# Optimization experiments

Measured on AMD Instinct MI355X. Metric: run time of the kernel, lower is better.

## Reference

```python
import jax, jax.numpy as jnp
import numpy as np

TEMPERATURE = 0.1
EPS = 1e-12  # F.normalize eps


def setup_inputs() -> dict:
    key = jax.random.key(0)
    k1, k2 = jax.random.split(key)
    B, D = 4096, 128
    return {
        "x_i": jax.random.normal(k1, (B, D), dtype=jnp.float32),
        "x_j": jax.random.normal(k2, (B, D), dtype=jnp.float32),
    }


def _l2_normalize(x):
    n = jnp.sqrt(jnp.sum(x * x, axis=1, keepdims=True))
    return x / jnp.maximum(n, EPS)


def reference(x_i, x_j):
    B = x_i.shape[0]
    z = jnp.concatenate([_l2_normalize(x_i), _l2_normalize(x_j)], axis=0)  # [2B, D]
    # cosine similarity of unit-norm rows == dot product -> single GEMM
    sim = z @ z.T  # [2B, 2B]
    idx = jnp.arange(B)
    sim_ij = sim[idx, idx + B]   # diag(sim, +B)
    sim_ji = sim[idx + B, idx]   # diag(sim, -B)
    positives = jnp.concatenate([sim_ij, sim_ji], axis=0)  # [2B]
    neg_mask = 1.0 - jnp.eye(2 * B, dtype=sim.dtype)
    denominator = jnp.sum(neg_mask * jnp.exp(sim / TEMPERATURE), axis=1)  # [2B]
    # -log(exp(pos/t) / denom) = -(pos/t - log denom)
    loss_partial = jnp.log(denominator) - positives / TEMPERATURE
    return jnp.sum(loss_partial) / (2 * B)
```

## Files before the change

### kernel.cpp

```cpp
#include <hip/hip_runtime.h>
#include <stdint.h>

#define D_DIM 128
#define NROW 8192
#define L2EPS 1e-12f
#define SCALE_A 14.426950408889634f
#define LN2 0.6931471805599453f
#define NPART 50

typedef __attribute__((ext_vector_type(4))) int   i32x4;
typedef __attribute__((ext_vector_type(8))) int   i32x8;
typedef __attribute__((ext_vector_type(4))) float f32x4;

#define AS1 __attribute__((address_space(1)))
#define AS3 __attribute__((address_space(3)))

static __device__ inline void gload_lds16(const void* g, void* l) {
    __builtin_amdgcn_global_load_lds((const AS1 uint32_t*)g, (AS3 uint32_t*)l, 16, 0, 0);
}

static __device__ inline i32x8 cat8(i32x4 lo, i32x4 hi) {
    i32x8 r;
    r[0] = lo[0]; r[1] = lo[1]; r[2] = lo[2]; r[3] = lo[3];
    r[4] = hi[0]; r[5] = hi[1]; r[6] = hi[2]; r[7] = hi[3];
    return r;
}

__global__ __launch_bounds__(256) void k_normalize(
        const float* __restrict__ xi, const float* __restrict__ xj,
        uint8_t* __restrict__ z8, uint8_t* __restrict__ z8s,
        float* __restrict__ pos_acc, float* __restrict__ logsum,
        unsigned* __restrict__ done_ct) {
    const int wave = threadIdx.x >> 6;
    const int lane = threadIdx.x & 63;
    const int row = blockIdx.x * 4 + wave;
    const float* src = (row < 4096) ? (xi + (size_t)row * D_DIM)
                                    : (xj + (size_t)(row - 4096) * D_DIM);
    float2 v = *(const float2*)(src + lane * 2);
    float ss = v.x * v.x + v.y * v.y;
#pragma unroll
    for (int m = 32; m >= 1; m >>= 1) ss += __shfl_xor(ss, m, 64);
    const float scale = 1.0f / fmaxf(sqrtf(ss), L2EPS);
    const float scale_a = scale * SCALE_A;
    const int pk_b = __builtin_amdgcn_cvt_pk_fp8_f32(v.x * scale,   v.y * scale,   0, false);
    const int pk_a = __builtin_amdgcn_cvt_pk_fp8_f32(v.x * scale_a, v.y * scale_a, 0, false);
    *(ushort*)(z8  + (size_t)row * D_DIM + lane * 2) = (ushort)pk_b;
    *(ushort*)(z8s + (size_t)row * D_DIM + lane * 2) = (ushort)pk_a;

    if (blockIdx.x == 0 && threadIdx.x == 0) {
        pos_acc[0] = 0.0f; logsum[0] = 0.0f; done_ct[0] = 0u;
    }
}

__global__ __launch_bounds__(256) void k_gemm(
        const uint8_t* __restrict__ z8, const uint8_t* __restrict__ z8s,
        float* __restrict__ part, float* __restrict__ pos_acc) {
    __shared__ __align__(16) uint8_t lds[32768];

    const int t = threadIdx.x;
    const int wave = t >> 6, lane = t & 63;
    const int quad = lane >> 4, lc = lane & 15;

    const int mb = blockIdx.x >> 6;
    const int rb = blockIdx.x & 63;
    const int rowbase = rb * 128;
    const bool diag = (mb == 16);
    const int c1 = diag ? rb : (rb + 2 * mb + 1) & 63;
    const int c2 = (rb + 2 * mb + 2) & 63;

    {
        const uint8_t* zb1 = z8 + (size_t)c1 * 128 * D_DIM;
#pragma unroll
        for (int q = 0; q < 4; q++) {
            const int s = q * 256 + t;
            const int r = s >> 3;
            const int g = (s & 7) ^ (r & 7);
            gload_lds16(zb1 + (size_t)r * D_DIM + g * 16, &lds[s * 16]);
        }
        if (!diag) {
            const uint8_t* zb2 = z8 + (size_t)c2 * 128 * D_DIM;
#pragma unroll
            for (int q = 0; q < 4; q++) {
                const int s = q * 256 + t;
                const int r = s >> 3;
                const int g = (s & 7) ^ (r & 7);
                gload_lds16(zb2 + (size_t)r * D_DIM + g * 16, &lds[16384 + s * 16]);
            }
        }
    }

    i32x8 afr[2];
    {
        const uint8_t* pa = z8s + (size_t)(rowbase + wave * 32 + lc) * D_DIM + quad * 32;
#pragma unroll
        for (int i = 0; i < 2; i++) {
            i32x4 lo = *(const i32x4*)(pa + i * 16 * D_DIM);
            i32x4 hi = *(const i32x4*)(pa + i * 16 * D_DIM + 16);
            afr[i] = cat8(lo, hi);
        }
    }

    asm volatile("s_waitcnt vmcnt(0)" ::: "memory");
    __syncthreads();

    float rs[2][4] = {{0.f,0.f,0.f,0.f},{0.f,0.f,0.f,0.f}};
    float cs[16];
#pragma unroll
    for (int j = 0; j < 16; j++) cs[j] = 0.f;
    float posp = 0.f;
    const int rl0 = wave * 32 + quad * 4;

#define MFMA_J(j, A0, A1)                                                     \
    i32x4 blo, bhi; {                                                         \
        const int rowb = ((j) * 16 + lc) * D_DIM;                             \
        blo = *(const i32x4*)&lds[rowb + (((quad * 2)     ^ (lc & 7)) * 16)]; \
        bhi = *(const i32x4*)&lds[rowb + (((quad * 2 + 1) ^ (lc & 7)) * 16)]; \
    }                                                                         \
    const i32x8 bfr = cat8(blo, bhi);                                         \
    f32x4 z4 = {0.f, 0.f, 0.f, 0.f};                                          \
    f32x4 A0 = __builtin_amdgcn_mfma_scale_f32_16x16x128_f8f6f4(              \
                   afr[0], bfr, z4, 0, 0, 0, 127, 0, 127);                    \
    f32x4 A1 = __builtin_amdgcn_mfma_scale_f32_16x16x128_f8f6f4(              \
                   afr[1], bfr, z4, 0, 0, 0, 127, 0, 127);

    if (!diag) {
#pragma unroll
        for (int j = 0; j < 8; j++) {
            MFMA_J(j, a0, a1)
#pragma unroll
            for (int r = 0; r < 4; r++) {
                const float e0 = exp2f(a0[r]);
                const float e1 = exp2f(a1[r]);
                rs[0][r] += e0;
                rs[1][r] += e1;
                cs[j] += e0 + e1;
            }
        }
        if (mb < 15) {
#pragma unroll
            for (int j = 8; j < 16; j++) {
                MFMA_J(j, a0, a1)
#pragma unroll
                for (int r = 0; r < 4; r++) {
                    const float e0 = exp2f(a0[r]);
                    const float e1 = exp2f(a1[r]);
                    rs[0][r] += e0;
                    rs[1][r] += e1;
                    cs[j] += e0 + e1;
                }
            }
        } else {
#pragma unroll
            for (int j = 8; j < 16; j++) {
                MFMA_J(j, a0, a1)
                const int clb = (j - 8) * 16 + lc;
#pragma unroll
                for (int i = 0; i < 2; i++)
#pragma unroll
                    for (int r = 0; r < 4; r++) {
                        const float s = (i ? a1 : a0)[r];
                        const float e = 0.5f * exp2f(s);
                        if (clb == rl0 + i * 16 + r) posp += s;
                        rs[i][r] += e;
                        cs[j] += e;
                    }
            }
        }
    } else {
#pragma unroll
        for (int j = 0; j < 8; j++) {
            MFMA_J(j, a0, a1)
            const int cl = j * 16 + lc;
#pragma unroll
            for (int i = 0; i < 2; i++)
#pragma unroll
                for (int r = 0; r < 4; r++) {
                    const float s = (i ? a1 : a0)[r];
                    const float e = (cl > rl0 + i * 16 + r) ? exp2f(s) : 0.f;
                    rs[i][r] += e;
                    cs[j] += e;
                }
        }
    }
#undef MFMA_J

#pragma unroll
    for (int i = 0; i < 2; i++)
#pragma unroll
        for (int r = 0; r < 4; r++) {
            float v = rs[i][r];
            v += __shfl_xor(v, 1, 64);
            v += __shfl_xor(v, 2, 64);
            v += __shfl_xor(v, 4, 64);
            v += __shfl_xor(v, 8, 64);
            if (lc == 0)
                part[(size_t)mb * NROW + rowbase + rl0 + i * 16 + r] = v;
        }

#pragma unroll
    for (int j = 0; j < 16; j++) {
        cs[j] += __shfl_xor(cs[j], 16, 64);
        cs[j] += __shfl_xor(cs[j], 32, 64);
    }
    __syncthreads();
    float* colred = (float*)lds;
    if (quad == 0) {
#pragma unroll
        for (int j = 0; j < 16; j++)
            colred[wave * 256 + j * 16 + lc] = cs[j];
    }
    __syncthreads();
    if (t < 256) {
        const float v = colred[t] + colred[256 + t] + colred[512 + t] + colred[768 + t];
        if (!diag) {
            const int slot = 17 + 2 * mb + (t >> 7);
            const int band = (t < 128) ? c1 : c2;
            part[(size_t)slot * NROW + band * 128 + (t & 127)] = v;
        } else if (t < 128) {
            part[(size_t)49 * NROW + c1 * 128 + t] = v;
        }
    }

    if (mb == 15) {
#pragma unroll
        for (int mm = 32; mm >= 1; mm >>= 1) posp += __shfl_xor(posp, mm, 64);
        if (lane == 0) atomicAdd(pos_acc, posp);
    }
}

__global__ __launch_bounds__(256) void k_logsum(
        const float* __restrict__ part, float* __restrict__ pos_acc,
        float* __restrict__ logsum, unsigned* __restrict__ done_ct,
        float* __restrict__ out) {
    const int row = blockIdx.x * 256 + threadIdx.x;
    float d = 0.f;
#pragma unroll
    for (int p = 0; p < NPART; p++) d += part[(size_t)p * NROW + row];
    float v = __logf(d);
#pragma unroll
    for (int m = 32; m >= 1; m >>= 1) v += __shfl_xor(v, m, 64);
    if ((threadIdx.x & 63) == 0) atomicAdd(logsum, v);
    __threadfence();
    __syncthreads();
    if (threadIdx.x == 0) {
        const unsigned prev = atomicAdd(done_ct, 1u);
        if (prev == gridDim.x - 1) {
            __threadfence();
            const float ls = atomicAdd(logsum, 0.0f);
            const float pp = atomicAdd(pos_acc, 0.0f);
            out[0] = (ls - pp * LN2) / (float)NROW;
        }
    }
}

extern "C" void kernel_launch(void* const* d_in, const int* in_sizes, int n_in,
                              void* d_out, int out_size, void* d_ws, size_t ws_size,
                              hipStream_t stream) {
    const float* xi = (const float*)d_in[0];
    const float* xj = (const float*)d_in[1];
    uint8_t* z8  = (uint8_t*)d_ws;
    uint8_t* z8s = z8 + (size_t)NROW * D_DIM;
    float* part = (float*)(z8s + (size_t)NROW * D_DIM);
    float* pos_acc = part + (size_t)NPART * NROW;
    float* logsum = pos_acc + 1;
    unsigned* done_ct = (unsigned*)(logsum + 1);
    float* out = (float*)d_out;

    hipLaunchKernelGGL(k_normalize, dim3(NROW / 4), dim3(256), 0, stream,
                       xi, xj, z8, z8s, pos_acc, logsum, done_ct);
    hipLaunchKernelGGL(k_gemm, dim3(17 * 64), dim3(256), 0, stream,
                       z8, z8s, part, pos_acc);
    hipLaunchKernelGGL(k_logsum, dim3(NROW / 256), dim3(256), 0, stream,
                       part, pos_acc, logsum, done_ct, out);
}
```

Baseline: 84.78 us.

## Fuse normalize, GEMM and log-sum into one kernel with grid-wide completion counter

Folds the separate normalize and log-sum kernels into the GEMM kernel. Each block now loads fp32 rows, normalizes them and quantizes them to fp8 straight into LDS and A fragments, so the fp8 workspace round trip disappears. The positive-pair sum and the log sum are reduced in two stages through small partial arrays, and the first 32 blocks spin-wait on an atomic counter before doing the final reduction. This removes two kernel launches but adds a memset launch, redundant normalization of each row by many blocks, and a spin-wait that assumes the waiting blocks cannot starve the blocks they wait on.

```diff
diff --git a/kernel.cpp b/kernel.cpp
--- a/kernel.cpp
+++ b/kernel.cpp
@@ -7,17 +7,11 @@
 #define SCALE_A 14.426950408889634f
 #define LN2 0.6931471805599453f
 #define NPART 50
+#define NBLK 1088
 
 typedef __attribute__((ext_vector_type(4))) int   i32x4;
 typedef __attribute__((ext_vector_type(8))) int   i32x8;
 typedef __attribute__((ext_vector_type(4))) float f32x4;
-
-#define AS1 __attribute__((address_space(1)))
-#define AS3 __attribute__((address_space(3)))
-
-static __device__ inline void gload_lds16(const void* g, void* l) {
-    __builtin_amdgcn_global_load_lds((const AS1 uint32_t*)g, (AS3 uint32_t*)l, 16, 0, 0);
-}
 
 static __device__ inline i32x8 cat8(i32x4 lo, i32x4 hi) {
     i32x8 r;
@@ -26,35 +20,41 @@
     return r;
 }
 
-__global__ __launch_bounds__(256) void k_normalize(
+static __device__ inline i32x4 pack16(const float* e, float sc) {
+    i32x4 u;
+#pragma unroll
+    for (int d = 0; d < 4; d++) {
+        int w = __builtin_amdgcn_cvt_pk_fp8_f32(e[4 * d] * sc, e[4 * d + 1] * sc, 0, false);
+        w = __builtin_amdgcn_cvt_pk_fp8_f32(e[4 * d + 2] * sc, e[4 * d + 3] * sc, w, true);
+        u[d] = w;
+    }
+    return u;
+}
+
+static __device__ inline float load_row32(const float* __restrict__ xi,
+                                          const float* __restrict__ xj,
+                                          int grow, int quad, float* e) {
+    const float* src = (grow < 4096) ? (xi + (size_t)grow * D_DIM)
+                                     : (xj + (size_t)(grow - 4096) * D_DIM);
+    const float* sq = src + quad * 32;
+    float ss = 0.f;
+#pragma unroll
+    for (int k2 = 0; k2 < 8; k2++) {
+        float4 v = *(const float4*)(sq + k2 * 4);
+        e[k2 * 4 + 0] = v.x; e[k2 * 4 + 1] = v.y;
+        e[k2 * 4 + 2] = v.z; e[k2 * 4 + 3] = v.w;
+        ss += v.x * v.x + v.y * v.y + v.z * v.z + v.w * v.w;
+    }
+    ss += __shfl_xor(ss, 16, 64);
+    ss += __shfl_xor(ss, 32, 64);
+    return ss;
+}
+
+__global__ __launch_bounds__(256) void k_all(
         const float* __restrict__ xi, const float* __restrict__ xj,
-        uint8_t* __restrict__ z8, uint8_t* __restrict__ z8s,
-        float* __restrict__ pos_acc, float* __restrict__ logsum,
-        unsigned* __restrict__ done_ct) {
-    const int wave = threadIdx.x >> 6;
-    const int lane = threadIdx.x & 63;
-    const int row = blockIdx.x * 4 + wave;
-    const float* src = (row < 4096) ? (xi + (size_t)row * D_DIM)
-                                    : (xj + (size_t)(row - 4096) * D_DIM);
-    float2 v = *(const float2*)(src + lane * 2);
-    float ss = v.x * v.x + v.y * v.y;
-#pragma unroll
-    for (int m = 32; m >= 1; m >>= 1) ss += __shfl_xor(ss, m, 64);
-    const float scale = 1.0f / fmaxf(sqrtf(ss), L2EPS);
-    const float scale_a = scale * SCALE_A;
-    const int pk_b = __builtin_amdgcn_cvt_pk_fp8_f32(v.x * scale,   v.y * scale,   0, false);
-    const int pk_a = __builtin_amdgcn_cvt_pk_fp8_f32(v.x * scale_a, v.y * scale_a, 0, false);
-    *(ushort*)(z8  + (size_t)row * D_DIM + lane * 2) = (ushort)pk_b;
-    *(ushort*)(z8s + (size_t)row * D_DIM + lane * 2) = (ushort)pk_a;
-
-    if (blockIdx.x == 0 && threadIdx.x == 0) {
-        pos_acc[0] = 0.0f; logsum[0] = 0.0f; done_ct[0] = 0u;
-    }
-}
-
-__global__ __launch_bounds__(256) void k_gemm(
-        const uint8_t* __restrict__ z8, const uint8_t* __restrict__ z8s,
-        float* __restrict__ part, float* __restrict__ pos_acc) {
+        float* __restrict__ part, float* __restrict__ pos_part,
+        float* __restrict__ ls_part, unsigned* __restrict__ done,
+        float* __restrict__ out) {
     __shared__ __align__(16) uint8_t lds[32768];
 
     const int t = threadIdx.x;
@@ -69,38 +69,32 @@
     const int c2 = (rb + 2 * mb + 2) & 63;
 
     {
-        const uint8_t* zb1 = z8 + (size_t)c1 * 128 * D_DIM;
-#pragma unroll
-        for (int q = 0; q < 4; q++) {
-            const int s = q * 256 + t;
-            const int r = s >> 3;
-            const int g = (s & 7) ^ (r & 7);
-            gload_lds16(zb1 + (size_t)r * D_DIM + g * 16, &lds[s * 16]);
-        }
-        if (!diag) {
-            const uint8_t* zb2 = z8 + (size_t)c2 * 128 * D_DIM;
-#pragma unroll
-            for (int q = 0; q < 4; q++) {
-                const int s = q * 256 + t;
-                const int r = s >> 3;
-                const int g = (s & 7) ^ (r & 7);
-                gload_lds16(zb2 + (size_t)r * D_DIM + g * 16, &lds[16384 + s * 16]);
-            }
+        const int nrr = diag ? 2 : 4;
+        for (int rr = 0; rr < nrr; rr++) {
+            const int rl = wave * (nrr * 16) + rr * 16 + lc;
+            const int band = (rl < 128) ? c1 : c2;
+            const int grow = band * 128 + (rl & 127);
+            float e[32];
+            const float ss = load_row32(xi, xj, grow, quad, e);
+            const float sc = 1.0f / fmaxf(sqrtf(ss), L2EPS);
+            const i32x4 u0 = pack16(e, sc);
+            const i32x4 u1 = pack16(e + 16, sc);
+            const int m7 = lc & 7;
+            *(i32x4*)&lds[rl * D_DIM + (((2 * quad)     ^ m7) * 16)] = u0;
+            *(i32x4*)&lds[rl * D_DIM + (((2 * quad + 1) ^ m7) * 16)] = u1;
         }
     }
 
     i32x8 afr[2];
-    {
-        const uint8_t* pa = z8s + (size_t)(rowbase + wave * 32 + lc) * D_DIM + quad * 32;
-#pragma unroll
-        for (int i = 0; i < 2; i++) {
-            i32x4 lo = *(const i32x4*)(pa + i * 16 * D_DIM);
-            i32x4 hi = *(const i32x4*)(pa + i * 16 * D_DIM + 16);
-            afr[i] = cat8(lo, hi);
-        }
-    }
-
-    asm volatile("s_waitcnt vmcnt(0)" ::: "memory");
+#pragma unroll
+    for (int i = 0; i < 2; i++) {
+        const int grow = rowbase + wave * 32 + i * 16 + lc;
+        float e[32];
+        const float ss = load_row32(xi, xj, grow, quad, e);
+        const float sc = SCALE_A / fmaxf(sqrtf(ss), L2EPS);
+        afr[i] = cat8(pack16(e, sc), pack16(e + 16, sc));
+    }
+
     __syncthreads();
 
     float rs[2][4] = {{0.f,0.f,0.f,0.f},{0.f,0.f,0.f,0.f}};
@@ -209,6 +203,11 @@
         for (int j = 0; j < 16; j++)
             colred[wave * 256 + j * 16 + lc] = cs[j];
     }
+    if (mb == 15) {
+#pragma unroll
+        for (int mm = 32; mm >= 1; mm >>= 1) posp += __shfl_xor(posp, mm, 64);
+        if (lane == 0) colred[1024 + wave] = posp;
+    }
     __syncthreads();
     if (t < 256) {
         const float v = colred[t] + colred[256 + t] + colred[512 + t] + colred[768 + t];
@@ -220,35 +219,45 @@
             part[(size_t)49 * NROW + c1 * 128 + t] = v;
         }
     }
-
-    if (mb == 15) {
-#pragma unroll
-        for (int mm = 32; mm >= 1; mm >>= 1) posp += __shfl_xor(posp, mm, 64);
-        if (lane == 0) atomicAdd(pos_acc, posp);
-    }
-}
-
-__global__ __launch_bounds__(256) void k_logsum(
-        const float* __restrict__ part, float* __restrict__ pos_acc,
-        float* __restrict__ logsum, unsigned* __restrict__ done_ct,
-        float* __restrict__ out) {
-    const int row = blockIdx.x * 256 + threadIdx.x;
-    float d = 0.f;
-#pragma unroll
-    for (int p = 0; p < NPART; p++) d += part[(size_t)p * NROW + row];
-    float v = __logf(d);
-#pragma unroll
-    for (int m = 32; m >= 1; m >>= 1) v += __shfl_xor(v, m, 64);
-    if ((threadIdx.x & 63) == 0) atomicAdd(logsum, v);
+    if (mb == 15 && t == 0)
+        pos_part[rb] = colred[1024] + colred[1025] + colred[1026] + colred[1027];
+
     __threadfence();
-    __syncthreads();
-    if (threadIdx.x == 0) {
-        const unsigned prev = atomicAdd(done_ct, 1u);
-        if (prev == gridDim.x - 1) {
+    if (t == 0) atomicAdd(&done[0], 1u);
+
+    if (blockIdx.x < 32) {
+        if (t == 0) {
+            while (__hip_atomic_load(&done[0], __ATOMIC_ACQUIRE,
+                                     __HIP_MEMORY_SCOPE_AGENT) < (unsigned)NBLK)
+                __builtin_amdgcn_s_sleep(2);
+        }
+        __syncthreads();
+        __threadfence();
+        const int row = blockIdx.x * 256 + t;
+        float d = 0.f;
+#pragma unroll
+        for (int p = 0; p < NPART; p++) d += part[(size_t)p * NROW + row];
+        float v = __logf(d);
+#pragma unroll
+        for (int m = 32; m >= 1; m >>= 1) v += __shfl_xor(v, m, 64);
+        __syncthreads();
+        if ((t & 63) == 0) ((float*)lds)[t >> 6] = v;
+        __syncthreads();
+        if (t == 0) {
+            float* f = (float*)lds;
+            ls_part[blockIdx.x] = f[0] + f[1] + f[2] + f[3];
             __threadfence();
-            const float ls = atomicAdd(logsum, 0.0f);
-            const float pp = atomicAdd(pos_acc, 0.0f);
-            out[0] = (ls - pp * LN2) / (float)NROW;
+            const unsigned prev = atomicAdd(&done[1], 1u);
+            if (prev == 31u) {
+                __threadfence();
+                float L = 0.f;
+#pragma unroll
+                for (int b = 0; b < 32; b++) L += ls_part[b];
+                float P = 0.f;
+#pragma unroll
+                for (int b = 0; b < 64; b++) P += pos_part[b];
+                out[0] = (L - P * LN2) / (float)NROW;
+            }
         }
     }
 }
@@ -258,18 +267,13 @@
                               hipStream_t stream) {
     const float* xi = (const float*)d_in[0];
     const float* xj = (const float*)d_in[1];
-    uint8_t* z8  = (uint8_t*)d_ws;
-    uint8_t* z8s = z8 + (size_t)NROW * D_DIM;
-    float* part = (float*)(z8s + (size_t)NROW * D_DIM);
-    float* pos_acc = part + (size_t)NPART * NROW;
-    float* logsum = pos_acc + 1;
-    unsigned* done_ct = (unsigned*)(logsum + 1);
+    float* part = (float*)d_ws;
+    float* pos_part = part + (size_t)NPART * NROW;
+    float* ls_part = pos_part + 64;
+    unsigned* done = (unsigned*)(ls_part + 32);
     float* out = (float*)d_out;
 
-    hipLaunchKernelGGL(k_normalize, dim3(NROW / 4), dim3(256), 0, stream,
-                       xi, xj, z8, z8s, pos_acc, logsum, done_ct);
-    hipLaunchKernelGGL(k_gemm, dim3(17 * 64), dim3(256), 0, stream,
-                       z8, z8s, part, pos_acc);
-    hipLaunchKernelGGL(k_logsum, dim3(NROW / 256), dim3(256), 0, stream,
-                       part, pos_acc, logsum, done_ct, out);
-}
+    hipMemsetAsync(done, 0, 2 * sizeof(unsigned), stream);
+    hipLaunchKernelGGL(k_all, dim3(NBLK), dim3(256), 0, stream,
+                       xi, xj, part, pos_part, ls_part, done, out);
+}
```

Result: slower. 194.9 us (+129.9%).
